# Performance work log

Measured on AMD Instinct MI355X. Metric: run time of the kernel, lower is better.

## Reference

```python
import jax, jax.numpy as jnp
import numpy as np

N_NODES = 100000
N_EDGES = 3200000


def _sage_conv(x, src, dst, Wl, Wr, b):
    # PyG SAGEConv (aggr='mean', root_weight=True, bias on lin_l):
    # out_i = mean_{j in N(i)} x_j @ Wl + x_i @ Wr + b
    msg = x[src]                                            # [E, F] gather
    s = jax.ops.segment_sum(msg, dst, num_segments=N_NODES)  # [N, F]
    cnt = jax.ops.segment_sum(jnp.ones((src.shape[0], 1), x.dtype), dst,
                              num_segments=N_NODES)          # [N, 1]
    agg = s / jnp.maximum(cnt, 1.0)                          # mean (0 for isolated nodes)
    return agg @ Wl + x @ Wr + b


def setup_inputs() -> dict:
    key = jax.random.key(0)
    ks = jax.random.split(key, 12)
    in_d, hid, out_d = 32, 24, 12
    x = jax.random.normal(ks[0], (N_NODES, in_d), dtype=jnp.float32)
    edge_index = jax.random.randint(ks[1], (2, N_EDGES), 0, N_NODES, dtype=jnp.int64)

    def glorot(k, fan_in, fan_out):
        lim = np.sqrt(6.0 / (fan_in + fan_out)).astype(np.float32)
        return jax.random.uniform(k, (fan_in, fan_out), jnp.float32, -lim, lim)

    return {
        "x": x,
        "edge_index": edge_index,
        "Wl1": glorot(ks[2], in_d, hid), "Wr1": glorot(ks[3], in_d, hid),
        "b1": jnp.zeros((hid,), jnp.float32),
        "Wl2": glorot(ks[4], hid, hid), "Wr2": glorot(ks[5], hid, hid),
        "b2": jnp.zeros((hid,), jnp.float32),
        "Wl3": glorot(ks[6], hid, out_d), "Wr3": glorot(ks[7], hid, out_d),
        "b3": jnp.zeros((out_d,), jnp.float32),
    }


def reference(x, edge_index, Wl1, Wr1, b1, Wl2, Wr2, b2, Wl3, Wr3, b3):
    src, dst = edge_index[0], edge_index[1]
    h = jax.nn.relu(_sage_conv(x, src, dst, Wl1, Wr1, b1))
    h = jax.nn.relu(_sage_conv(h, src, dst, Wl2, Wr2, b2))
    h = jax.nn.sigmoid(_sage_conv(h, src, dst, Wl3, Wr3, b3))
    return h
```

## Files before the change

### kernel.cpp

```cpp
#include <hip/hip_runtime.h>
#include <cstdint>
#include <cstddef>

#define NT 256
constexpr int SHIFT  = 7;
constexpr int NBK    = 1024;
constexpr int BMASK  = (1 << SHIFT) - 1;
constexpr int EPB    = 12800;
constexpr int TSPLIT = 50000;

__device__ __forceinline__ float sigf(float v) {
    return 1.0f / (1.0f + __expf(-v));
}
__device__ __forceinline__ float bf2f(unsigned short u) {
    return __uint_as_float((unsigned)u << 16);
}
__device__ __forceinline__ unsigned short f2bf(float f) {
    unsigned u = __float_as_uint(f);
    return (unsigned short)((u + 0x7fffu + ((u >> 16) & 1u)) >> 16);
}


__global__ __launch_bounds__(NT)
void p1_k(const int* __restrict__ dst, int* __restrict__ cnts, int e_total, int nPB)
{
    __shared__ int h[NBK];
    for (int i = threadIdx.x; i < NBK; i += NT) h[i] = 0;
    __syncthreads();
    int base = blockIdx.x * EPB;
    for (int it = 0; it < EPB / NT; ++it) {
        int e = base + it * NT + threadIdx.x;
        if (e < e_total) atomicAdd(&h[dst[e] >> SHIFT], 1);
    }
    __syncthreads();
    for (int b = threadIdx.x; b < NBK; b += NT)
        cnts[b * nPB + blockIdx.x] = h[b];
}

__global__ __launch_bounds__(NT)
void scan1_k(int* data, int* __restrict__ bsum, int n)
{
    __shared__ int s[NT];
    int t = threadIdx.x;
    int i = blockIdx.x * NT + t;
    int v = (i < n) ? data[i] : 0;
    s[t] = v;
    __syncthreads();
    for (int off = 1; off < NT; off <<= 1) {
        int add = (t >= off) ? s[t - off] : 0;
        __syncthreads();
        s[t] += add;
        __syncthreads();
    }
    if (i < n) data[i] = s[t] - v;
    if (t == NT - 1) bsum[blockIdx.x] = s[t];
}

__global__ __launch_bounds__(1024)
void scan2_k(int* bsum, int* __restrict__ boff, int nb)
{
    __shared__ int s[1024];
    int t = threadIdx.x;
    int v = (t < nb) ? bsum[t] : 0;
    s[t] = v;
    __syncthreads();
    for (int off = 1; off < 1024; off <<= 1) {
        int add = (t >= off) ? s[t - off] : 0;
        __syncthreads();
        s[t] += add;
        __syncthreads();
    }
    if (t < nb) boff[t] = s[t] - v;
}

__global__ __launch_bounds__(NT)
void p2_k(const int* __restrict__ src, const int* __restrict__ dst,
          const int* __restrict__ ecnts, const int* __restrict__ boff,
          unsigned* __restrict__ part, int e_total, int nPB)
{
    __shared__ int gb[NBK];
    __shared__ int cur[NBK];
    for (int i = threadIdx.x; i < NBK; i += NT) {
        int g = i * nPB + blockIdx.x;
        gb[i]  = ecnts[g] + boff[g / NT];
        cur[i] = 0;
    }
    __syncthreads();
    int base = blockIdx.x * EPB;
    for (int it = 0; it < EPB / NT; ++it) {
        int e = base + it * NT + threadIdx.x;
        if (e < e_total) {
            int d = dst[e];
            int s = src[e];
            int b = d >> SHIFT;
            int r = atomicAdd(&cur[b], 1);
            part[gb[b] + r] = ((unsigned)s << SHIFT) | (unsigned)(d & BMASK);
        }
    }
}

__global__ __launch_bounds__(NT)
void b_k(const unsigned* __restrict__ part, const int* __restrict__ ecnts,
         const int* __restrict__ boff, int* __restrict__ row_ptr,
         int* __restrict__ mptr, int* __restrict__ col,
         int nPB, int n, int e_total)
{
    constexpr int NB2 = 1 << SHIFT;
    __shared__ int d0[NB2], dt[NB2], sc[NB2], c0[NB2], c1[NB2];
    const int b = blockIdx.x;
    const int t = threadIdx.x;
    int g0 = b * nPB;
    const int e0 = ecnts[g0] + boff[g0 / NT];
    int g1 = (b + 1) * nPB;
    const int e1 = ecnts[g1] + boff[g1 / NT];

    if (t < NB2) { d0[t] = 0; dt[t] = 0; }
    __syncthreads();
    for (int e = e0 + t; e < e1; e += NT) {
        unsigned p = part[e];
        int l = p & BMASK;
        int s = (int)(p >> SHIFT);
        atomicAdd(&dt[l], 1);
        if (s < TSPLIT) atomicAdd(&d0[l], 1);
    }
    __syncthreads();
    if (t < NB2) sc[t] = dt[t];
    __syncthreads();
    for (int off = 1; off < NB2; off <<= 1) {
        int add = (t >= off && t < NB2) ? sc[t - off] : 0;
        __syncthreads();
        if (t < NB2) sc[t] += add;
        __syncthreads();
    }
    if (t < NB2) {
        int excl = sc[t] - dt[t];
        int st0  = e0 + excl;
        int node = (b << SHIFT) + t;
        if (node <= n) row_ptr[node] = st0;
        if (node <  n) mptr[node]    = st0 + d0[t];
        c0[t] = st0;
        c1[t] = st0 + d0[t];
    }
    __syncthreads();
    for (int e = e0 + t; e < e1; e += NT) {
        unsigned p = part[e];
        int l = p & BMASK;
        int s = (int)(p >> SHIFT);
        int* cp = (s < TSPLIT) ? &c0[l] : &c1[l];
        int pos = atomicAdd(cp, 1);
        col[pos] = s;
    }
}

__global__ __launch_bounds__(NT)
void cvt_k(const float* __restrict__ x, unsigned short* __restrict__ xb, int ntot)
{
    int i = blockIdx.x * NT + threadIdx.x;
    if (i < ntot) xb[i] = f2bf(x[i]);
}

__global__ __launch_bounds__(NT)
void gA_k(const unsigned short* __restrict__ Hin, const int* __restrict__ row_ptr,
          const int* __restrict__ mptr, const int* __restrict__ col,
          float* __restrict__ P, int n)
{
    const int lane8 = threadIdx.x & 7;
    const int grp   = threadIdx.x >> 3;
    const int node  = blockIdx.x * (NT / 8) + grp;
    if (node >= n) return;
    const int e0 = row_ptr[node];
    const int e1 = mptr[node];
    const ushort4* rows = reinterpret_cast<const ushort4*>(Hin);
    float a0 = 0.f, a1 = 0.f, a2 = 0.f, a3 = 0.f;
    int e = e0;
    for (; e + 3 < e1; e += 4) {
        int s0 = col[e], s1 = col[e + 1], s2 = col[e + 2], s3 = col[e + 3];
        ushort4 v0 = rows[(size_t)s0 * 8 + lane8];
        ushort4 v1 = rows[(size_t)s1 * 8 + lane8];
        ushort4 v2 = rows[(size_t)s2 * 8 + lane8];
        ushort4 v3 = rows[(size_t)s3 * 8 + lane8];
        a0 += bf2f(v0.x) + bf2f(v1.x) + bf2f(v2.x) + bf2f(v3.x);
        a1 += bf2f(v0.y) + bf2f(v1.y) + bf2f(v2.y) + bf2f(v3.y);
        a2 += bf2f(v0.z) + bf2f(v1.z) + bf2f(v2.z) + bf2f(v3.z);
        a3 += bf2f(v0.w) + bf2f(v1.w) + bf2f(v2.w) + bf2f(v3.w);
    }
    for (; e < e1; ++e) {
        ushort4 v0 = rows[(size_t)col[e] * 8 + lane8];
        a0 += bf2f(v0.x); a1 += bf2f(v0.y); a2 += bf2f(v0.z); a3 += bf2f(v0.w);
    }
    reinterpret_cast<float4*>(P + (size_t)node * 32)[lane8] = make_float4(a0, a1, a2, a3);
}

template<int FIN, int FOUT, int ACT>
__global__ __launch_bounds__(NT)
void gB_k(const unsigned short* __restrict__ Hin, const int* __restrict__ row_ptr,
          const int* __restrict__ mptr, const int* __restrict__ col,
          const float* __restrict__ P, const float* __restrict__ Wl,
          const float* __restrict__ Wr, const float* __restrict__ b,
          void* __restrict__ Hout, int n)
{
    constexpr int FS  = 32;
    constexpr int NPB = NT / 8;
    constexpr int GS  = 2 * FS + 4;
    __shared__ float sm[NPB * GS];

    const int lane8 = threadIdx.x & 7;
    const int grp   = threadIdx.x >> 3;
    const int node  = blockIdx.x * NPB + grp;
    const bool valid = node < n;

    if (valid) {
        const int rp0 = row_ptr[node];
        const int rpm = mptr[node];
        const int rp1 = row_ptr[node + 1];
        const ushort4* rows = reinterpret_cast<const ushort4*>(Hin);
        float4 pv = reinterpret_cast<const float4*>(P + (size_t)node * 32)[lane8];
        float a0 = pv.x, a1 = pv.y, a2 = pv.z, a3 = pv.w;
        ushort4 xv = rows[(size_t)node * 8 + lane8];
        int e = rpm;
        for (; e + 3 < rp1; e += 4) {
            int s0 = col[e], s1 = col[e + 1], s2 = col[e + 2], s3 = col[e + 3];
            ushort4 v0 = rows[(size_t)s0 * 8 + lane8];
            ushort4 v1 = rows[(size_t)s1 * 8 + lane8];
            ushort4 v2 = rows[(size_t)s2 * 8 + lane8];
            ushort4 v3 = rows[(size_t)s3 * 8 + lane8];
            a0 += bf2f(v0.x) + bf2f(v1.x) + bf2f(v2.x) + bf2f(v3.x);
            a1 += bf2f(v0.y) + bf2f(v1.y) + bf2f(v2.y) + bf2f(v3.y);
            a2 += bf2f(v0.z) + bf2f(v1.z) + bf2f(v2.z) + bf2f(v3.z);
            a3 += bf2f(v0.w) + bf2f(v1.w) + bf2f(v2.w) + bf2f(v3.w);
        }
        for (; e < rp1; ++e) {
            ushort4 v0 = rows[(size_t)col[e] * 8 + lane8];
            a0 += bf2f(v0.x); a1 += bf2f(v0.y); a2 += bf2f(v0.z); a3 += bf2f(v0.w);
        }
        float invd = 1.0f / fmaxf((float)(rp1 - rp0), 1.0f);
        float* smg = sm + grp * GS;
        smg[4 * lane8 + 0]      = a0 * invd;
        smg[4 * lane8 + 1]      = a1 * invd;
        smg[4 * lane8 + 2]      = a2 * invd;
        smg[4 * lane8 + 3]      = a3 * invd;
        smg[FS + 4 * lane8 + 0] = bf2f(xv.x);
        smg[FS + 4 * lane8 + 1] = bf2f(xv.y);
        smg[FS + 4 * lane8 + 2] = bf2f(xv.z);
        smg[FS + 4 * lane8 + 3] = bf2f(xv.w);
    }
    __syncthreads();

    if (!valid) return;
    const float* smg = sm + grp * GS;

    if constexpr (ACT == 0) {
        unsigned short* out = (unsigned short*)Hout + (size_t)node * FS;
#pragma unroll
        for (int j = 0; j < 4; ++j) {
            int f = lane8 + 8 * j;
            float r = 0.0f;
            if (f < FOUT) {
                float a = b[f];
#pragma unroll
                for (int k = 0; k < FIN; ++k) {
                    a = fmaf(smg[k],      Wl[k * FOUT + f], a);
                    a = fmaf(smg[FS + k], Wr[k * FOUT + f], a);
                }
                r = fmaxf(a, 0.0f);
            }
            out[f] = f2bf(r);
        }
    } else {
        float* out = (float*)Hout + (size_t)node * FOUT;
#pragma unroll
        for (int j = 0; j < (FOUT + 7) / 8; ++j) {
            int f = lane8 + 8 * j;
            if (f < FOUT) {
                float a = b[f];
#pragma unroll
                for (int k = 0; k < FIN; ++k) {
                    a = fmaf(smg[k],      Wl[k * FOUT + f], a);
                    a = fmaf(smg[FS + k], Wr[k * FOUT + f], a);
                }
                out[f] = sigf(a);
            }
        }
    }
}

extern "C" void kernel_launch(void* const* d_in, const int* in_sizes, int n_in,
                              void* d_out, int out_size, void* d_ws, size_t ws_size,
                              hipStream_t stream)
{
    const float* x   = (const float*)d_in[0];
    const int*   ei  = (const int*)d_in[1];
    const float* Wl1 = (const float*)d_in[2];
    const float* Wr1 = (const float*)d_in[3];
    const float* b1  = (const float*)d_in[4];
    const float* Wl2 = (const float*)d_in[5];
    const float* Wr2 = (const float*)d_in[6];
    const float* b2  = (const float*)d_in[7];
    const float* Wl3 = (const float*)d_in[8];
    const float* Wr3 = (const float*)d_in[9];
    const float* b3  = (const float*)d_in[10];

    const int N = in_sizes[0] / 32;
    const int E = in_sizes[1] / 2;
    const int* src = ei;
    const int* dst = ei + E;

    const int nPB = (E + EPB - 1) / EPB;
    const int M   = NBK * nPB;
    const int nSB = (M + NT - 1) / NT;
    const int nBK = ((N - 1) >> SHIFT) + 1;
    const int nbG = (N + 31) / 32;
    const int nbC = (N * 32 + NT - 1) / NT;

    int* row_ptr = (int*)d_ws;
    int* cnts    = row_ptr + (N + 2);
    int* bsum    = cnts + M;
    int* boff    = bsum + 1024;
    int* mptr    = boff + 1024;
    size_t off   = (size_t)(N + 2) + M + 2048 + N;
    off = (off + 3) & ~(size_t)3;
    int* col     = (int*)d_ws + off;
    off += E;
    unsigned* part = (unsigned*)((int*)d_ws + off);
    float*    P    = (float*)part;
    off += E;
    unsigned short* xb  = (unsigned short*)((int*)d_ws + off);
    unsigned short* H1b = xb  + (size_t)N * 32;
    unsigned short* H2b = H1b + (size_t)N * 32;

    p1_k   <<<nPB, NT,   0, stream>>>(dst, cnts, E, nPB);
    scan1_k<<<nSB, NT,   0, stream>>>(cnts, bsum, M);
    scan2_k<<<1,   1024, 0, stream>>>(bsum, boff, nSB);
    p2_k   <<<nPB, NT,   0, stream>>>(src, dst, cnts, boff, part, E, nPB);
    b_k    <<<nBK, NT,   0, stream>>>(part, cnts, boff, row_ptr, mptr, col, nPB, N, E);

    cvt_k  <<<nbC, NT,   0, stream>>>(x, xb, N * 32);

    gA_k            <<<nbG, NT, 0, stream>>>(xb,  row_ptr, mptr, col, P, N);
    gB_k<32, 24, 0> <<<nbG, NT, 0, stream>>>(xb,  row_ptr, mptr, col, P, Wl1, Wr1, b1, H1b, N);
    gA_k            <<<nbG, NT, 0, stream>>>(H1b, row_ptr, mptr, col, P, N);
    gB_k<24, 24, 0> <<<nbG, NT, 0, stream>>>(H1b, row_ptr, mptr, col, P, Wl2, Wr2, b2, H2b, N);
    gA_k            <<<nbG, NT, 0, stream>>>(H2b, row_ptr, mptr, col, P, N);
    gB_k<24, 12, 1> <<<nbG, NT, 0, stream>>>(H2b, row_ptr, mptr, col, P, Wl3, Wr3, b3, (float*)d_out, N);
}
```

Baseline: 263.3 us.

## Fuse histogram and scatter into one block-local partition kernel with LDS staging

Replaces the global count/scan/scatter sequence (p1, scan1, scan2, p2) with a single kernel per edge chunk. Each chunk builds its histogram, scans it locally, sorts its edges into LDS, and writes them back contiguously, recording per-bucket run starts and counts plus global bucket totals via atomics. The CSR build kernel then walks each bucket's runs (one thread per run) using a tiny global scan of the totals. This removes two launches and a full extra read of dst and makes the partition writes coalesced. In exchange it needs about 50KB of LDS per block, which limits occupancy, and the per-thread serial run loops in b_k are poorly coalesced.

```diff
diff --git a/kernel.cpp b/kernel.cpp
--- a/kernel.cpp
+++ b/kernel.cpp
@@ -20,48 +20,75 @@
     return (unsigned short)((u + 0x7fffu + ((u >> 16) & 1u)) >> 16);
 }
 
-
-__global__ __launch_bounds__(NT)
-void p1_k(const int* __restrict__ dst, int* __restrict__ cnts, int e_total, int nPB)
-{
-    __shared__ int h[NBK];
-    for (int i = threadIdx.x; i < NBK; i += NT) h[i] = 0;
-    __syncthreads();
-    int base = blockIdx.x * EPB;
-    for (int it = 0; it < EPB / NT; ++it) {
-        int e = base + it * NT + threadIdx.x;
-        if (e < e_total) atomicAdd(&h[dst[e] >> SHIFT], 1);
-    }
-    __syncthreads();
-    for (int b = threadIdx.x; b < NBK; b += NT)
-        cnts[b * nPB + blockIdx.x] = h[b];
-}
-
-__global__ __launch_bounds__(NT)
-void scan1_k(int* data, int* __restrict__ bsum, int n)
-{
-    __shared__ int s[NT];
-    int t = threadIdx.x;
-    int i = blockIdx.x * NT + t;
-    int v = (i < n) ? data[i] : 0;
-    s[t] = v;
+__global__ __launch_bounds__(NT)
+void part_k(const int* __restrict__ src, const int* __restrict__ dst,
+            unsigned* __restrict__ part, int* __restrict__ runstart,
+            int* __restrict__ runcnt, int* __restrict__ totcnt,
+            int e_total, int nPB)
+{
+    __shared__ unsigned stage[EPB];
+    __shared__ int hist[NBK];
+    __shared__ int curs[NBK];
+    __shared__ int tsum[NT];
+    const int b    = blockIdx.x;
+    const int t    = threadIdx.x;
+    const int base = b * EPB;
+    const int nh   = min(EPB, e_total - base);
+
+    for (int i = t; i < NBK; i += NT) hist[i] = 0;
+    __syncthreads();
+    for (int i = t; i < nh; i += NT)
+        atomicAdd(&hist[dst[base + i] >> SHIFT], 1);
+    __syncthreads();
+
+    const int f0 = 4 * t;
+    int h0 = hist[f0], h1 = hist[f0 + 1], h2 = hist[f0 + 2], h3 = hist[f0 + 3];
+    int incl = h0 + h1 + h2 + h3;
+    tsum[t] = incl;
     __syncthreads();
     for (int off = 1; off < NT; off <<= 1) {
-        int add = (t >= off) ? s[t - off] : 0;
-        __syncthreads();
-        s[t] += add;
-        __syncthreads();
-    }
-    if (i < n) data[i] = s[t] - v;
-    if (t == NT - 1) bsum[blockIdx.x] = s[t];
+        int add = (t >= off) ? tsum[t - off] : 0;
+        __syncthreads();
+        tsum[t] += add;
+        __syncthreads();
+    }
+    int ex = tsum[t] - incl;
+    curs[f0]     = ex;
+    curs[f0 + 1] = ex + h0;
+    curs[f0 + 2] = ex + h0 + h1;
+    curs[f0 + 3] = ex + h0 + h1 + h2;
+    runstart[(f0    ) * nPB + b] = base + ex;
+    runstart[(f0 + 1) * nPB + b] = base + ex + h0;
+    runstart[(f0 + 2) * nPB + b] = base + ex + h0 + h1;
+    runstart[(f0 + 3) * nPB + b] = base + ex + h0 + h1 + h2;
+    runcnt[(f0    ) * nPB + b] = h0;
+    runcnt[(f0 + 1) * nPB + b] = h1;
+    runcnt[(f0 + 2) * nPB + b] = h2;
+    runcnt[(f0 + 3) * nPB + b] = h3;
+    if (h0) atomicAdd(&totcnt[f0],     h0);
+    if (h1) atomicAdd(&totcnt[f0 + 1], h1);
+    if (h2) atomicAdd(&totcnt[f0 + 2], h2);
+    if (h3) atomicAdd(&totcnt[f0 + 3], h3);
+    __syncthreads();
+
+    for (int i = t; i < nh; i += NT) {
+        int d = dst[base + i];
+        int s = src[base + i];
+        int f = d >> SHIFT;
+        int r = atomicAdd(&curs[f], 1);
+        stage[r] = ((unsigned)s << SHIFT) | (unsigned)(d & BMASK);
+    }
+    __syncthreads();
+
+    for (int i = t; i < nh; i += NT) part[base + i] = stage[i];
 }
 
 __global__ __launch_bounds__(1024)
-void scan2_k(int* bsum, int* __restrict__ boff, int nb)
+void tscan_k(const int* __restrict__ totcnt, int* __restrict__ fbase)
 {
     __shared__ int s[1024];
     int t = threadIdx.x;
-    int v = (t < nb) ? bsum[t] : 0;
+    int v = totcnt[t];
     s[t] = v;
     __syncthreads();
     for (int off = 1; off < 1024; off <<= 1) {
@@ -70,60 +97,33 @@
         s[t] += add;
         __syncthreads();
     }
-    if (t < nb) boff[t] = s[t] - v;
-}
-
-__global__ __launch_bounds__(NT)
-void p2_k(const int* __restrict__ src, const int* __restrict__ dst,
-          const int* __restrict__ ecnts, const int* __restrict__ boff,
-          unsigned* __restrict__ part, int e_total, int nPB)
-{
-    __shared__ int gb[NBK];
-    __shared__ int cur[NBK];
-    for (int i = threadIdx.x; i < NBK; i += NT) {
-        int g = i * nPB + blockIdx.x;
-        gb[i]  = ecnts[g] + boff[g / NT];
-        cur[i] = 0;
-    }
-    __syncthreads();
-    int base = blockIdx.x * EPB;
-    for (int it = 0; it < EPB / NT; ++it) {
-        int e = base + it * NT + threadIdx.x;
-        if (e < e_total) {
-            int d = dst[e];
-            int s = src[e];
-            int b = d >> SHIFT;
-            int r = atomicAdd(&cur[b], 1);
-            part[gb[b] + r] = ((unsigned)s << SHIFT) | (unsigned)(d & BMASK);
-        }
-    }
-}
-
-__global__ __launch_bounds__(NT)
-void b_k(const unsigned* __restrict__ part, const int* __restrict__ ecnts,
-         const int* __restrict__ boff, int* __restrict__ row_ptr,
-         int* __restrict__ mptr, int* __restrict__ col,
-         int nPB, int n, int e_total)
+    fbase[t] = s[t] - v;
+}
+
+__global__ __launch_bounds__(NT)
+void b_k(const unsigned* __restrict__ part, const int* __restrict__ runstart,
+         const int* __restrict__ runcnt, const int* __restrict__ fbase,
+         int* __restrict__ row_ptr, int* __restrict__ mptr,
+         int* __restrict__ col, int nPB, int n)
 {
     constexpr int NB2 = 1 << SHIFT;
     __shared__ int d0[NB2], dt[NB2], sc[NB2], c0[NB2], c1[NB2];
-    const int b = blockIdx.x;
+    const int f = blockIdx.x;
     const int t = threadIdx.x;
-    int g0 = b * nPB;
-    const int e0 = ecnts[g0] + boff[g0 / NT];
-    int g1 = (b + 1) * nPB;
-    const int e1 = ecnts[g1] + boff[g1 / NT];
-
+
+    int rs = 0, rc = 0;
+    if (t < nPB) { rs = runstart[f * nPB + t]; rc = runcnt[f * nPB + t]; }
     if (t < NB2) { d0[t] = 0; dt[t] = 0; }
     __syncthreads();
-    for (int e = e0 + t; e < e1; e += NT) {
-        unsigned p = part[e];
+
+    for (int i = 0; i < rc; ++i) {
+        unsigned p = part[rs + i];
         int l = p & BMASK;
-        int s = (int)(p >> SHIFT);
         atomicAdd(&dt[l], 1);
-        if (s < TSPLIT) atomicAdd(&d0[l], 1);
-    }
-    __syncthreads();
+        if ((int)(p >> SHIFT) < TSPLIT) atomicAdd(&d0[l], 1);
+    }
+    __syncthreads();
+
     if (t < NB2) sc[t] = dt[t];
     __syncthreads();
     for (int off = 1; off < NB2; off <<= 1) {
@@ -134,20 +134,20 @@
     }
     if (t < NB2) {
         int excl = sc[t] - dt[t];
-        int st0  = e0 + excl;
-        int node = (b << SHIFT) + t;
+        int st0  = fbase[f] + excl;
+        int node = (f << SHIFT) + t;
         if (node <= n) row_ptr[node] = st0;
         if (node <  n) mptr[node]    = st0 + d0[t];
         c0[t] = st0;
         c1[t] = st0 + d0[t];
     }
     __syncthreads();
-    for (int e = e0 + t; e < e1; e += NT) {
-        unsigned p = part[e];
+
+    for (int i = 0; i < rc; ++i) {
+        unsigned p = part[rs + i];
         int l = p & BMASK;
         int s = (int)(p >> SHIFT);
-        int* cp = (s < TSPLIT) ? &c0[l] : &c1[l];
-        int pos = atomicAdd(cp, 1);
+        int pos = atomicAdd((s < TSPLIT) ? &c0[l] : &c1[l], 1);
         col[pos] = s;
     }
 }
@@ -306,20 +306,19 @@
     const int* dst = ei + E;
 
     const int nPB = (E + EPB - 1) / EPB;
-    const int M   = NBK * nPB;
-    const int nSB = (M + NT - 1) / NT;
     const int nBK = ((N - 1) >> SHIFT) + 1;
     const int nbG = (N + 31) / 32;
     const int nbC = (N * 32 + NT - 1) / NT;
 
-    int* row_ptr = (int*)d_ws;
-    int* cnts    = row_ptr + (N + 2);
-    int* bsum    = cnts + M;
-    int* boff    = bsum + 1024;
-    int* mptr    = boff + 1024;
-    size_t off   = (size_t)(N + 2) + M + 2048 + N;
+    int* runstart = (int*)d_ws;
+    int* runcnt   = runstart + (size_t)NBK * nPB;
+    int* totcnt   = runcnt + (size_t)NBK * nPB;
+    int* fbase    = totcnt + 1024;
+    int* row_ptr  = fbase + 1024;
+    int* mptr     = row_ptr + (N + 2);
+    size_t off    = 2 * (size_t)NBK * nPB + 2048 + (N + 2) + N;
     off = (off + 3) & ~(size_t)3;
-    int* col     = (int*)d_ws + off;
+    int* col      = (int*)d_ws + off;
     off += E;
     unsigned* part = (unsigned*)((int*)d_ws + off);
     float*    P    = (float*)part;
@@ -328,11 +327,11 @@
     unsigned short* H1b = xb  + (size_t)N * 32;
     unsigned short* H2b = H1b + (size_t)N * 32;
 
-    p1_k   <<<nPB, NT,   0, stream>>>(dst, cnts, E, nPB);
-    scan1_k<<<nSB, NT,   0, stream>>>(cnts, bsum, M);
-    scan2_k<<<1,   1024, 0, stream>>>(bsum, boff, nSB);
-    p2_k   <<<nPB, NT,   0, stream>>>(src, dst, cnts, boff, part, E, nPB);
-    b_k    <<<nBK, NT,   0, stream>>>(part, cnts, boff, row_ptr, mptr, col, nPB, N, E);
+    hipMemsetAsync(totcnt, 0, 1024 * sizeof(int), stream);
+
+    part_k <<<nPB, NT,   0, stream>>>(src, dst, part, runstart, runcnt, totcnt, E, nPB);
+    tscan_k<<<1,   1024, 0, stream>>>(totcnt, fbase);
+    b_k    <<<nBK, NT,   0, stream>>>(part, runstart, runcnt, fbase, row_ptr, mptr, col, nPB, N);
 
     cvt_k  <<<nbC, NT,   0, stream>>>(x, xb, N * 32);
 
```

Result: slower. 328.7 us (+24.8%).
